# Optimization experiments

Hardware: AMD Instinct MI355X
Metric: run time of the kernel (lower is better)

Reference implementation:

```python
import jax, jax.numpy as jnp
import numpy as np

N_NODES = 50000
N_GRAPHS = 64


def _gcn_layer(x, w, b, src, dst, dinv):
    # GCNConv: out = D^{-1/2} (A+I) D^{-1/2} (x W) + b; self-loops already in src/dst
    xw = x @ w                                  # [N, out]
    norm = (dinv[src] * dinv[dst])[:, None]     # [E+N, 1]
    msgs = xw[src] * norm                       # gather + scale
    out = jax.ops.segment_sum(msgs, dst, num_segments=N_NODES)
    return out + b


def setup_inputs() -> dict:
    key = jax.random.key(0)
    ks = jax.random.split(key, 12)
    E = 800000
    F_IN, H = 128, 256
    x = jax.random.normal(ks[0], (N_NODES, F_IN), dtype=jnp.float32)
    edge_attr = jax.random.normal(ks[1], (E, 4), dtype=jnp.float32)
    edge_index = jax.random.randint(ks[2], (2, E), 0, N_NODES, dtype=jnp.int64)
    batch = jnp.sort(jax.random.randint(ks[3], (N_NODES,), 0, N_GRAPHS, dtype=jnp.int64))
    def glorot(k, fi, fo):
        s = jnp.sqrt(6.0 / (fi + fo))
        return jax.random.uniform(k, (fi, fo), minval=-s, maxval=s, dtype=jnp.float32)
    return {
        "x": x, "edge_attr": edge_attr, "edge_index": edge_index, "batch": batch,
        "w1": glorot(ks[4], F_IN, H), "b1": jnp.zeros((H,), jnp.float32),
        "w2": glorot(ks[5], H, H), "b2": jnp.zeros((H,), jnp.float32),
        "w3": glorot(ks[6], H, H), "b3": jnp.zeros((H,), jnp.float32),
        "lin1_w": glorot(ks[7], H, H // 2), "lin1_b": jnp.zeros((H // 2,), jnp.float32),
        "lin2_w": glorot(ks[8], H // 2, 3), "lin2_b": jnp.zeros((3,), jnp.float32),
    }


def reference(x, edge_attr, edge_index, batch, w1, b1, w2, b2, w3, b3,
              lin1_w, lin1_b, lin2_w, lin2_b):
    # add self-loops once; shared by all three conv layers
    loop = jnp.arange(N_NODES, dtype=edge_index.dtype)
    src = jnp.concatenate([edge_index[0], loop])
    dst = jnp.concatenate([edge_index[1], loop])
    deg = jax.ops.segment_sum(jnp.ones_like(dst, dtype=x.dtype), dst, num_segments=N_NODES)
    dinv = jnp.where(deg > 0, jax.lax.rsqrt(deg), 0.0)

    h = jax.nn.relu(_gcn_layer(x, w1, b1, src, dst, dinv))
    h = jax.nn.relu(_gcn_layer(h, w2, b2, src, dst, dinv))
    h = _gcn_layer(h, w3, b3, src, dst, dinv)

    # global mean pool over graphs
    sums = jax.ops.segment_sum(h, batch, num_segments=N_GRAPHS)
    cnts = jax.ops.segment_sum(jnp.ones((h.shape[0],), h.dtype), batch, num_segments=N_GRAPHS)
    pooled = sums / jnp.maximum(cnts, 1.0)[:, None]

    # eval mode: dropout is identity
    out = pooled @ lin1_w + lin1_b
    out = out @ lin2_w + lin2_b
    return out
```

## Files before the change

### kernel.cpp

```cpp
#include <hip/hip_runtime.h>
#include <cstdint>

constexpr int NG = 64;
constexpr int H  = 256;

typedef __bf16 bf16x8 __attribute__((ext_vector_type(8)));
typedef float  f32x4  __attribute__((ext_vector_type(4)));

__device__ __forceinline__ uint32_t pk_bf16(float a, float b) {
    uint32_t ua = __builtin_bit_cast(uint32_t, a);
    uint32_t ub = __builtin_bit_cast(uint32_t, b);
    ua += 0x7fffu + ((ua >> 16) & 1u);
    ub += 0x7fffu + ((ub >> 16) & 1u);
    return (ua >> 16) | (ub & 0xffff0000u);
}
__device__ __forceinline__ ushort bf16r(float x) {
    uint32_t u = __builtin_bit_cast(uint32_t, x);
    u += 0x7fffu + ((u >> 16) & 1u);
    return (ushort)(u >> 16);
}
__device__ __forceinline__ float bf2f(ushort h) {
    return __builtin_bit_cast(float, ((uint32_t)h) << 16);
}
__device__ __forceinline__ void bf2acc(uint32_t u, float& a0, float& a1) {
    a0 += __builtin_bit_cast(float, u << 16);
    a1 += __builtin_bit_cast(float, u & 0xffff0000u);
}

__global__ void hist_kernel(const int* __restrict__ dst, int* __restrict__ cnt, int E) {
    int e = blockIdx.x * blockDim.x + threadIdx.x;
    if (e < E) atomicAdd(&cnt[dst[e]], 1);
}

__global__ void dinv_kernel(const int* __restrict__ cnt, float* __restrict__ dinv, int n) {
    int i = blockIdx.x * blockDim.x + threadIdx.x;
    if (i < n) dinv[i] = rsqrtf((float)(cnt[i] + 1));
}

__global__ __launch_bounds__(256) void scanA(const int* __restrict__ cnt, int* __restrict__ bsum, int n) {
    __shared__ int sh[256];
    int t = threadIdx.x, i = blockIdx.x * 256 + t;
    sh[t] = (i < n) ? cnt[i] : 0;
    __syncthreads();
    for (int off = 128; off > 0; off >>= 1) {
        if (t < off) sh[t] += sh[t + off];
        __syncthreads();
    }
    if (t == 0) bsum[blockIdx.x] = sh[0];
}

__global__ __launch_bounds__(256) void scanB(const int* __restrict__ bsum, int* __restrict__ boff,
                                             int* __restrict__ total_out, int nb) {
    __shared__ int sh[256];
    int t = threadIdx.x;
    int v = (t < nb) ? bsum[t] : 0;
    sh[t] = v;
    __syncthreads();
    for (int off = 1; off < 256; off <<= 1) {
        int a = (t >= off) ? sh[t - off] : 0;
        __syncthreads();
        sh[t] += a;
        __syncthreads();
    }
    if (t < nb) boff[t] = sh[t] - v;
    if (t == nb - 1) *total_out = sh[t];
}

__global__ __launch_bounds__(256) void scanC(const int* __restrict__ cnt, const int* __restrict__ boff,
                                             int* __restrict__ row_ptr, int* __restrict__ fill, int n) {
    __shared__ int sh[256];
    int t = threadIdx.x, i = blockIdx.x * 256 + t;
    int v = (i < n) ? cnt[i] : 0;
    sh[t] = v;
    __syncthreads();
    for (int off = 1; off < 256; off <<= 1) {
        int a = (t >= off) ? sh[t - off] : 0;
        __syncthreads();
        sh[t] += a;
        __syncthreads();
    }
    if (i < n) {
        int excl = boff[blockIdx.x] + sh[t] - v;
        row_ptr[i] = excl;
        fill[i] = excl;
    }
}

__global__ void scatter_kernel(const int* __restrict__ src, const int* __restrict__ dst,
                               int* __restrict__ fill, int* __restrict__ ssrc, int E) {
    int e = blockIdx.x * blockDim.x + threadIdx.x;
    if (e < E) {
        int pos = atomicAdd(&fill[dst[e]], 1);
        ssrc[pos] = src[e];
    }
}

__global__ void wconv_kernel(const float* __restrict__ w, ushort* __restrict__ hi,
                             ushort* __restrict__ lo, int K) {
    int idx = blockIdx.x * 256 + threadIdx.x;
    if (idx >= K * 256) return;
    int k = idx >> 8, n = idx & 255;
    float v = w[idx];
    ushort h = bf16r(v);
    float r = v - bf2f(h);
    hi[n * K + k] = h;
    lo[n * K + k] = bf16r(r);
}

__global__ void prescale_kernel(const float* __restrict__ x, const float* __restrict__ dinv,
                                ushort* __restrict__ y, int total) {
    int idx = blockIdx.x * blockDim.x + threadIdx.x;
    int f = idx * 4;
    if (f >= total) return;
    float dv = dinv[f >> 7];
    float4 v = *reinterpret_cast<const float4*>(x + f);
    uint2 o;
    o.x = pk_bf16(v.x * dv, v.y * dv);
    o.y = pk_bf16(v.z * dv, v.w * dv);
    *reinterpret_cast<uint2*>(y + f) = o;
}

template<int VEC>
__global__ __launch_bounds__(256) void agg_kernel(const ushort* __restrict__ y,
                                                  const float* __restrict__ dinv,
                                                  const int* __restrict__ row_ptr,
                                                  const int* __restrict__ ssrc,
                                                  ushort* __restrict__ zout, int n) {
    constexpr int W = VEC * 64;
    int wave = threadIdx.x >> 6;
    int lane = threadIdx.x & 63;
    int node = blockIdx.x * 4 + wave;
    if (node >= n) return;
    float acc[VEC] = {};

    auto ld4 = [&](int s) -> uint2 {
        return *reinterpret_cast<const uint2*>(y + (size_t)s * W + lane * VEC);
    };
    auto ld2 = [&](int s) -> uint32_t {
        return *reinterpret_cast<const uint32_t*>(y + (size_t)s * W + lane * VEC);
    };

    if constexpr (VEC == 4) {
        uint2 v = ld4(node);
        bf2acc(v.x, acc[0], acc[1]); bf2acc(v.y, acc[2], acc[3]);
    } else {
        bf2acc(ld2(node), acc[0], acc[1]);
    }

    int beg = row_ptr[node], end = row_ptr[node + 1];
    int e = beg;
    for (; e + 4 <= end; e += 4) {
        int s0 = ssrc[e], s1 = ssrc[e + 1], s2 = ssrc[e + 2], s3 = ssrc[e + 3];
        if constexpr (VEC == 4) {
            uint2 v0 = ld4(s0), v1 = ld4(s1), v2 = ld4(s2), v3 = ld4(s3);
            bf2acc(v0.x, acc[0], acc[1]); bf2acc(v0.y, acc[2], acc[3]);
            bf2acc(v1.x, acc[0], acc[1]); bf2acc(v1.y, acc[2], acc[3]);
            bf2acc(v2.x, acc[0], acc[1]); bf2acc(v2.y, acc[2], acc[3]);
            bf2acc(v3.x, acc[0], acc[1]); bf2acc(v3.y, acc[2], acc[3]);
        } else {
            uint32_t v0 = ld2(s0), v1 = ld2(s1), v2 = ld2(s2), v3 = ld2(s3);
            bf2acc(v0, acc[0], acc[1]); bf2acc(v1, acc[0], acc[1]);
            bf2acc(v2, acc[0], acc[1]); bf2acc(v3, acc[0], acc[1]);
        }
    }
    for (; e < end; ++e) {
        if constexpr (VEC == 4) {
            uint2 v = ld4(ssrc[e]);
            bf2acc(v.x, acc[0], acc[1]); bf2acc(v.y, acc[2], acc[3]);
        } else {
            bf2acc(ld2(ssrc[e]), acc[0], acc[1]);
        }
    }

    float dv = dinv[node];
    ushort* zp = zout + (size_t)node * W + lane * VEC;
    if constexpr (VEC == 4) {
        uint2 o;
        o.x = pk_bf16(dv * acc[0], dv * acc[1]);
        o.y = pk_bf16(dv * acc[2], dv * acc[3]);
        *reinterpret_cast<uint2*>(zp) = o;
    } else {
        *reinterpret_cast<uint32_t*>(zp) = pk_bf16(dv * acc[0], dv * acc[1]);
    }
}

template<bool RELU>
__global__ __launch_bounds__(256) void mfma_gemm(const ushort* __restrict__ A,
                                                 const ushort* __restrict__ Bhi,
                                                 const ushort* __restrict__ Blo,
                                                 const float* __restrict__ bias,
                                                 const float* __restrict__ dinv,
                                                 ushort* __restrict__ C, int M, int K) {
    constexpr int BM = 64, BN = 64, BK = 64;
    constexpr int LDK = BK + 8;
    __shared__ ushort As[BM][LDK];
    __shared__ ushort Bh[BN][LDK];
    __shared__ ushort Bl[BN][LDK];

    const int tid = threadIdx.x;
    const int w = tid >> 6;
    const int l = tid & 63;
    const int lr = l & 15;
    const int lk = (l >> 4) * 8;
    const int bm = blockIdx.x * BM;
    const int bn = blockIdx.y * BN;

    f32x4 acc[4];
    #pragma unroll
    for (int i = 0; i < 4; ++i) acc[i] = (f32x4){0.f, 0.f, 0.f, 0.f};

    for (int k0 = 0; k0 < K; k0 += BK) {
        #pragma unroll
        for (int p = 0; p < 2; ++p) {
            int g = tid + p * 256;
            int r = g >> 3;
            int c = (g & 7) << 3;
            int grow = bm + r;
            uint4 va = make_uint4(0u, 0u, 0u, 0u);
            if (grow < M) va = *reinterpret_cast<const uint4*>(A + (size_t)grow * K + k0 + c);
            *reinterpret_cast<uint4*>(&As[r][c]) = va;
            *reinterpret_cast<uint4*>(&Bh[r][c]) =
                *reinterpret_cast<const uint4*>(Bhi + (size_t)(bn + r) * K + k0 + c);
            *reinterpret_cast<uint4*>(&Bl[r][c]) =
                *reinterpret_cast<const uint4*>(Blo + (size_t)(bn + r) * K + k0 + c);
        }
        __syncthreads();
        #pragma unroll
        for (int kk = 0; kk < BK; kk += 32) {
            bf16x8 bh = *reinterpret_cast<const bf16x8*>(&Bh[w * 16 + lr][kk + lk]);
            bf16x8 bl = *reinterpret_cast<const bf16x8*>(&Bl[w * 16 + lr][kk + lk]);
            #pragma unroll
            for (int r16 = 0; r16 < 4; ++r16) {
                bf16x8 a = *reinterpret_cast<const bf16x8*>(&As[r16 * 16 + lr][kk + lk]);
                acc[r16] = __builtin_amdgcn_mfma_f32_16x16x32_bf16(a, bh, acc[r16], 0, 0, 0);
                acc[r16] = __builtin_amdgcn_mfma_f32_16x16x32_bf16(a, bl, acc[r16], 0, 0, 0);
            }
        }
        __syncthreads();
    }

    int col = bn + w * 16 + lr;
    float bv = bias[col];
    #pragma unroll
    for (int r16 = 0; r16 < 4; ++r16) {
        #pragma unroll
        for (int j = 0; j < 4; ++j) {
            int row = bm + r16 * 16 + (l >> 4) * 4 + j;
            if (row < M) {
                float v = acc[r16][j] + bv;
                if (RELU) v = fmaxf(v, 0.f);
                v *= dinv[row];
                C[(size_t)row * H + col] = bf16r(v);
            }
        }
    }
}

__global__ __launch_bounds__(256) void pool_kernel(const ushort* __restrict__ z,
                                                   const int* __restrict__ batch,
                                                   float* __restrict__ sums,
                                                   int* __restrict__ gcnt, int n) {
    constexpr int NCH = 128;
    int t = threadIdx.x;
    int base = blockIdx.x * NCH;
    if (base >= n) return;
    int endn = min(base + NCH, n);
    int cur = batch[base];
    float local = 0.f;
    int cl = 0;
    for (int i = base; i < endn; ++i) {
        int g = batch[i];
        if (g != cur) {
            atomicAdd(&sums[cur * H + t], local);
            if (t == 0) atomicAdd(&gcnt[cur], cl);
            local = 0.f; cl = 0; cur = g;
        }
        local += bf2f(z[(size_t)i * H + t]);
        cl++;
    }
    atomicAdd(&sums[cur * H + t], local);
    if (t == 0) atomicAdd(&gcnt[cur], cl);
}

__global__ __launch_bounds__(256) void head_kernel(const float* __restrict__ sums,
                                                   const int* __restrict__ gcnt,
                                                   const float* __restrict__ w3, const float* __restrict__ b3,
                                                   const float* __restrict__ l1w, const float* __restrict__ l1b,
                                                   const float* __restrict__ l2w, const float* __restrict__ l2b,
                                                   float* __restrict__ out) {
    __shared__ float pooled[H];
    __shared__ float t3[H];
    __shared__ float mid[H / 2];
    int g = blockIdx.x, t = threadIdx.x;
    float c = (float)max(gcnt[g], 1);
    pooled[t] = sums[g * H + t] / c;
    __syncthreads();
    float a = b3[t];
    for (int k = 0; k < H; ++k) a += pooled[k] * w3[k * H + t];
    t3[t] = a;
    __syncthreads();
    if (t < H / 2) {
        float m = l1b[t];
        for (int k = 0; k < H; ++k) m += t3[k] * l1w[k * (H / 2) + t];
        mid[t] = m;
    }
    __syncthreads();
    if (t < 3) {
        float o = l2b[t];
        for (int k = 0; k < H / 2; ++k) o += mid[k] * l2w[k * 3 + t];
        out[g * 3 + t] = o;
    }
}

extern "C" void kernel_launch(void* const* d_in, const int* in_sizes, int n_in,
                              void* d_out, int out_size, void* d_ws, size_t ws_size,
                              hipStream_t stream) {
    const float* x   = (const float*)d_in[0];
    const int*   ei  = (const int*)d_in[2];
    const int*   bat = (const int*)d_in[3];
    const float* w1  = (const float*)d_in[4];
    const float* b1  = (const float*)d_in[5];
    const float* w2  = (const float*)d_in[6];
    const float* b2  = (const float*)d_in[7];
    const float* w3  = (const float*)d_in[8];
    const float* b3  = (const float*)d_in[9];
    const float* l1w = (const float*)d_in[10];
    const float* l1b = (const float*)d_in[11];
    const float* l2w = (const float*)d_in[12];
    const float* l2b = (const float*)d_in[13];
    float* out = (float*)d_out;

    const int N = in_sizes[0] / 128;
    const int E = in_sizes[2] / 2;
    const int NB = (N + 255) / 256;

    char* ws = (char*)d_ws;
    size_t off = 0;
    auto alloc = [&](size_t bytes) {
        void* p = ws + off;
        off = (off + bytes + 255) & ~(size_t)255;
        return p;
    };
    ushort* yb     = (ushort*)alloc((size_t)N * H * 2);
    ushort* z16    = (ushort*)alloc((size_t)N * H * 2);
    int*    cnt    = (int*)alloc((size_t)N * 4);
    float*  dinv   = (float*)alloc((size_t)N * 4);
    int*    row_ptr= (int*)alloc((size_t)(N + 1) * 4);
    int*    fill   = (int*)alloc((size_t)N * 4);
    int*    ssrc   = (int*)alloc((size_t)E * 4);
    int*    bsum   = (int*)alloc(256 * 4);
    int*    boff   = (int*)alloc(256 * 4);
    ushort* wt1h   = (ushort*)alloc((size_t)128 * 256 * 2);
    ushort* wt1l   = (ushort*)alloc((size_t)128 * 256 * 2);
    ushort* wt2h   = (ushort*)alloc((size_t)256 * 256 * 2);
    ushort* wt2l   = (ushort*)alloc((size_t)256 * 256 * 2);
    float*  sums   = (float*)alloc((size_t)NG * H * 4);
    int*    gcnt   = (int*)alloc((size_t)NG * 4);

    hipMemsetAsync(cnt, 0, (size_t)N * 4, stream);
    hipMemsetAsync(sums, 0, (size_t)NG * H * 4, stream);
    hipMemsetAsync(gcnt, 0, (size_t)NG * 4, stream);

    hist_kernel<<<(E + 255) / 256, 256, 0, stream>>>(ei + E, cnt, E);
    dinv_kernel<<<(N + 255) / 256, 256, 0, stream>>>(cnt, dinv, N);
    scanA<<<NB, 256, 0, stream>>>(cnt, bsum, N);
    scanB<<<1, 256, 0, stream>>>(bsum, boff, row_ptr + N, NB);
    scanC<<<NB, 256, 0, stream>>>(cnt, boff, row_ptr, fill, N);
    scatter_kernel<<<(E + 255) / 256, 256, 0, stream>>>(ei, ei + E, fill, ssrc, E);

    wconv_kernel<<<(128 * 256) / 256, 256, 0, stream>>>(w1, wt1h, wt1l, 128);
    wconv_kernel<<<(256 * 256) / 256, 256, 0, stream>>>(w2, wt2h, wt2l, 256);

    prescale_kernel<<<(N * 128 / 4 + 255) / 256, 256, 0, stream>>>(x, dinv, yb, N * 128);
    agg_kernel<2><<<(N + 3) / 4, 256, 0, stream>>>(yb, dinv, row_ptr, ssrc, z16, N);
    mfma_gemm<true><<<dim3((N + 63) / 64, 4), 256, 0, stream>>>(z16, wt1h, wt1l, b1, dinv, yb, N, 128);

    agg_kernel<4><<<(N + 3) / 4, 256, 0, stream>>>(yb, dinv, row_ptr, ssrc, z16, N);
    mfma_gemm<true><<<dim3((N + 63) / 64, 4), 256, 0, stream>>>(z16, wt2h, wt2l, b2, dinv, yb, N, 256);

    agg_kernel<4><<<(N + 3) / 4, 256, 0, stream>>>(yb, dinv, row_ptr, ssrc, z16, N);

    pool_kernel<<<(N + 127) / 128, 256, 0, stream>>>(z16, bat, sums, gcnt, N);
    head_kernel<<<NG, 256, 0, stream>>>(sums, gcnt, w3, b3, l1w, l1b, l2w, l2b, out);
}
```

Measured before the change: 486.0 us.

## Fuse preprocessing kernels, deepen aggregation unroll, and enlarge GEMM row tile

The inverse-degree computation moves into the first scan kernel. Edge scatter and input prescaling share one launch, and the two weight conversions become a single launch, which cuts kernel launches and extra passes over small arrays. The neighbour-gather loop in aggregation gains an 8-way unrolled stage so more independent gathers are in flight per wave. The MFMA GEMM row tile grows from 64 to 128 to reuse the B tiles more, at the cost of more accumulator registers and LDS per block, which may lower occupancy.

```diff
diff --git a/kernel.cpp b/kernel.cpp
--- a/kernel.cpp
+++ b/kernel.cpp
@@ -32,15 +32,13 @@
     if (e < E) atomicAdd(&cnt[dst[e]], 1);
 }
 
-__global__ void dinv_kernel(const int* __restrict__ cnt, float* __restrict__ dinv, int n) {
-    int i = blockIdx.x * blockDim.x + threadIdx.x;
-    if (i < n) dinv[i] = rsqrtf((float)(cnt[i] + 1));
-}
-
-__global__ __launch_bounds__(256) void scanA(const int* __restrict__ cnt, int* __restrict__ bsum, int n) {
+__global__ __launch_bounds__(256) void scanA(const int* __restrict__ cnt, int* __restrict__ bsum,
+                                             float* __restrict__ dinv, int n) {
     __shared__ int sh[256];
     int t = threadIdx.x, i = blockIdx.x * 256 + t;
-    sh[t] = (i < n) ? cnt[i] : 0;
+    int v = (i < n) ? cnt[i] : 0;
+    if (i < n) dinv[i] = rsqrtf((float)(v + 1));
+    sh[t] = v;
     __syncthreads();
     for (int off = 128; off > 0; off >>= 1) {
         if (t < off) sh[t] += sh[t + off];
@@ -86,38 +84,38 @@
     }
 }
 
-__global__ void scatter_kernel(const int* __restrict__ src, const int* __restrict__ dst,
-                               int* __restrict__ fill, int* __restrict__ ssrc, int E) {
-    int e = blockIdx.x * blockDim.x + threadIdx.x;
-    if (e < E) {
-        int pos = atomicAdd(&fill[dst[e]], 1);
-        ssrc[pos] = src[e];
-    }
-}
-
-__global__ void wconv_kernel(const float* __restrict__ w, ushort* __restrict__ hi,
-                             ushort* __restrict__ lo, int K) {
+__global__ void sp_kernel(const int* __restrict__ src, const int* __restrict__ dst,
+                          int* __restrict__ fill, int* __restrict__ ssrc, int E,
+                          const float* __restrict__ x, const float* __restrict__ dinv,
+                          ushort* __restrict__ y, int np4 ) {
+    int i = blockIdx.x * blockDim.x + threadIdx.x;
+    if (i < E) {
+        int pos = atomicAdd(&fill[dst[i]], 1);
+        ssrc[pos] = src[i];
+    }
+    if (i < np4) {
+        int f = i * 4;
+        float dv = dinv[f >> 7];
+        float4 v = *reinterpret_cast<const float4*>(x + f);
+        uint2 o;
+        o.x = pk_bf16(v.x * dv, v.y * dv);
+        o.y = pk_bf16(v.z * dv, v.w * dv);
+        *reinterpret_cast<uint2*>(y + f) = o;
+    }
+}
+
+__global__ void wconv_kernel(const float* __restrict__ w1, ushort* __restrict__ h1, ushort* __restrict__ l1,
+                             const float* __restrict__ w2, ushort* __restrict__ h2, ushort* __restrict__ l2) {
     int idx = blockIdx.x * 256 + threadIdx.x;
-    if (idx >= K * 256) return;
-    int k = idx >> 8, n = idx & 255;
+    const float* w; ushort *hi, *lo; int K;
+    if (idx < 128 * 256) { w = w1; hi = h1; lo = l1; K = 128; }
+    else { idx -= 128 * 256; if (idx >= 256 * 256) return; w = w2; hi = h2; lo = l2; K = 256; }
+    int k = idx / 256, n = idx & 255;
     float v = w[idx];
     ushort h = bf16r(v);
     float r = v - bf2f(h);
     hi[n * K + k] = h;
     lo[n * K + k] = bf16r(r);
-}
-
-__global__ void prescale_kernel(const float* __restrict__ x, const float* __restrict__ dinv,
-                                ushort* __restrict__ y, int total) {
-    int idx = blockIdx.x * blockDim.x + threadIdx.x;
-    int f = idx * 4;
-    if (f >= total) return;
-    float dv = dinv[f >> 7];
-    float4 v = *reinterpret_cast<const float4*>(x + f);
-    uint2 o;
-    o.x = pk_bf16(v.x * dv, v.y * dv);
-    o.y = pk_bf16(v.z * dv, v.w * dv);
-    *reinterpret_cast<uint2*>(y + f) = o;
 }
 
 template<int VEC>
@@ -149,18 +147,44 @@
 
     int beg = row_ptr[node], end = row_ptr[node + 1];
     int e = beg;
+    for (; e + 8 <= end; e += 8) {
+        int s[8];
+        #pragma unroll
+        for (int q = 0; q < 8; ++q) s[q] = ssrc[e + q];
+        if constexpr (VEC == 4) {
+            uint2 v[8];
+            #pragma unroll
+            for (int q = 0; q < 8; ++q) v[q] = ld4(s[q]);
+            #pragma unroll
+            for (int q = 0; q < 8; ++q) {
+                bf2acc(v[q].x, acc[0], acc[1]); bf2acc(v[q].y, acc[2], acc[3]);
+            }
+        } else {
+            uint32_t v[8];
+            #pragma unroll
+            for (int q = 0; q < 8; ++q) v[q] = ld2(s[q]);
+            #pragma unroll
+            for (int q = 0; q < 8; ++q) bf2acc(v[q], acc[0], acc[1]);
+        }
+    }
     for (; e + 4 <= end; e += 4) {
-        int s0 = ssrc[e], s1 = ssrc[e + 1], s2 = ssrc[e + 2], s3 = ssrc[e + 3];
+        int s[4];
+        #pragma unroll
+        for (int q = 0; q < 4; ++q) s[q] = ssrc[e + q];
         if constexpr (VEC == 4) {
-            uint2 v0 = ld4(s0), v1 = ld4(s1), v2 = ld4(s2), v3 = ld4(s3);
-            bf2acc(v0.x, acc[0], acc[1]); bf2acc(v0.y, acc[2], acc[3]);
-            bf2acc(v1.x, acc[0], acc[1]); bf2acc(v1.y, acc[2], acc[3]);
-            bf2acc(v2.x, acc[0], acc[1]); bf2acc(v2.y, acc[2], acc[3]);
-            bf2acc(v3.x, acc[0], acc[1]); bf2acc(v3.y, acc[2], acc[3]);
+            uint2 v[4];
+            #pragma unroll
+            for (int q = 0; q < 4; ++q) v[q] = ld4(s[q]);
+            #pragma unroll
+            for (int q = 0; q < 4; ++q) {
+                bf2acc(v[q].x, acc[0], acc[1]); bf2acc(v[q].y, acc[2], acc[3]);
+            }
         } else {
-            uint32_t v0 = ld2(s0), v1 = ld2(s1), v2 = ld2(s2), v3 = ld2(s3);
-            bf2acc(v0, acc[0], acc[1]); bf2acc(v1, acc[0], acc[1]);
-            bf2acc(v2, acc[0], acc[1]); bf2acc(v3, acc[0], acc[1]);
+            uint32_t v[4];
+            #pragma unroll
+            for (int q = 0; q < 4; ++q) v[q] = ld2(s[q]);
+            #pragma unroll
+            for (int q = 0; q < 4; ++q) bf2acc(v[q], acc[0], acc[1]);
         }
     }
     for (; e < end; ++e) {
@@ -191,7 +215,7 @@
                                                  const float* __restrict__ bias,
                                                  const float* __restrict__ dinv,
                                                  ushort* __restrict__ C, int M, int K) {
-    constexpr int BM = 64, BN = 64, BK = 64;
+    constexpr int BM = 128, BN = 64, BK = 64;
     constexpr int LDK = BK + 8;
     __shared__ ushort As[BM][LDK];
     __shared__ ushort Bh[BN][LDK];
@@ -205,13 +229,13 @@
     const int bm = blockIdx.x * BM;
     const int bn = blockIdx.y * BN;
 
-    f32x4 acc[4];
+    f32x4 acc[8];
     #pragma unroll
-    for (int i = 0; i < 4; ++i) acc[i] = (f32x4){0.f, 0.f, 0.f, 0.f};
+    for (int i = 0; i < 8; ++i) acc[i] = (f32x4){0.f, 0.f, 0.f, 0.f};
 
     for (int k0 = 0; k0 < K; k0 += BK) {
         #pragma unroll
-        for (int p = 0; p < 2; ++p) {
+        for (int p = 0; p < 4; ++p) {
             int g = tid + p * 256;
             int r = g >> 3;
             int c = (g & 7) << 3;
@@ -219,6 +243,12 @@
             uint4 va = make_uint4(0u, 0u, 0u, 0u);
             if (grow < M) va = *reinterpret_cast<const uint4*>(A + (size_t)grow * K + k0 + c);
             *reinterpret_cast<uint4*>(&As[r][c]) = va;
+        }
+        #pragma unroll
+        for (int p = 0; p < 2; ++p) {
+            int g = tid + p * 256;
+            int r = g >> 3;
+            int c = (g & 7) << 3;
             *reinterpret_cast<uint4*>(&Bh[r][c]) =
                 *reinterpret_cast<const uint4*>(Bhi + (size_t)(bn + r) * K + k0 + c);
             *reinterpret_cast<uint4*>(&Bl[r][c]) =
@@ -230,7 +260,7 @@
             bf16x8 bh = *reinterpret_cast<const bf16x8*>(&Bh[w * 16 + lr][kk + lk]);
             bf16x8 bl = *reinterpret_cast<const bf16x8*>(&Bl[w * 16 + lr][kk + lk]);
             #pragma unroll
-            for (int r16 = 0; r16 < 4; ++r16) {
+            for (int r16 = 0; r16 < 8; ++r16) {
                 bf16x8 a = *reinterpret_cast<const bf16x8*>(&As[r16 * 16 + lr][kk + lk]);
                 acc[r16] = __builtin_amdgcn_mfma_f32_16x16x32_bf16(a, bh, acc[r16], 0, 0, 0);
                 acc[r16] = __builtin_amdgcn_mfma_f32_16x16x32_bf16(a, bl, acc[r16], 0, 0, 0);
@@ -242,7 +272,7 @@
     int col = bn + w * 16 + lr;
     float bv = bias[col];
     #pragma unroll
-    for (int r16 = 0; r16 < 4; ++r16) {
+    for (int r16 = 0; r16 < 8; ++r16) {
         #pragma unroll
         for (int j = 0; j < 4; ++j) {
             int row = bm + r16 * 16 + (l >> 4) * 4 + j;
@@ -362,21 +392,18 @@
     hipMemsetAsync(gcnt, 0, (size_t)NG * 4, stream);
 
     hist_kernel<<<(E + 255) / 256, 256, 0, stream>>>(ei + E, cnt, E);
-    dinv_kernel<<<(N + 255) / 256, 256, 0, stream>>>(cnt, dinv, N);
-    scanA<<<NB, 256, 0, stream>>>(cnt, bsum, N);
+    scanA<<<NB, 256, 0, stream>>>(cnt, bsum, dinv, N);
     scanB<<<1, 256, 0, stream>>>(bsum, boff, row_ptr + N, NB);
     scanC<<<NB, 256, 0, stream>>>(cnt, boff, row_ptr, fill, N);
-    scatter_kernel<<<(E + 255) / 256, 256, 0, stream>>>(ei, ei + E, fill, ssrc, E);
-
-    wconv_kernel<<<(128 * 256) / 256, 256, 0, stream>>>(w1, wt1h, wt1l, 128);
-    wconv_kernel<<<(256 * 256) / 256, 256, 0, stream>>>(w2, wt2h, wt2l, 256);
-
-    prescale_kernel<<<(N * 128 / 4 + 255) / 256, 256, 0, stream>>>(x, dinv, yb, N * 128);
+    wconv_kernel<<<(128 * 256 + 256 * 256) / 256, 256, 0, stream>>>(w1, wt1h, wt1l, w2, wt2h, wt2l);
+    sp_kernel<<<(N * 32 + 255) / 256, 256, 0, stream>>>(ei, ei + E, fill, ssrc, E,
+                                                        x, dinv, yb, N * 32);
+
     agg_kernel<2><<<(N + 3) / 4, 256, 0, stream>>>(yb, dinv, row_ptr, ssrc, z16, N);
-    mfma_gemm<true><<<dim3((N + 63) / 64, 4), 256, 0, stream>>>(z16, wt1h, wt1l, b1, dinv, yb, N, 128);
+    mfma_gemm<true><<<dim3((N + 127) / 128, 4), 256, 0, stream>>>(z16, wt1h, wt1l, b1, dinv, yb, N, 128);
 
     agg_kernel<4><<<(N + 3) / 4, 256, 0, stream>>>(yb, dinv, row_ptr, ssrc, z16, N);
-    mfma_gemm<true><<<dim3((N + 63) / 64, 4), 256, 0, stream>>>(z16, wt2h, wt2l, b2, dinv, yb, N, 256);
+    mfma_gemm<true><<<dim3((N + 127) / 128, 4), 256, 0, stream>>>(z16, wt2h, wt2l, b2, dinv, yb, N, 256);
 
     agg_kernel<4><<<(N + 3) / 4, 256, 0, stream>>>(yb, dinv, row_ptr, ssrc, z16, N);
 
```

Measured after the change: 470.0 us. 1.03x faster.
